# Kernel optimization log

Hardware: AMD Instinct MI355X
Metric: run time of the kernel (lower is better)

## Reference

```python
import jax, jax.numpy as jnp
import numpy as np

N, E, IN_DIM, H, D = 50000, 1600000, 128, 8, 16


def setup_inputs() -> dict:
    key = jax.random.key(0)
    ks = jax.random.split(key, 9)
    s = 1.0 / np.sqrt(IN_DIM)
    return {
        "h": jax.random.normal(ks[0], (N, IN_DIM), dtype=jnp.float32),
        "Wq": jax.random.normal(ks[1], (IN_DIM, H * D), dtype=jnp.float32) * s,
        "bq": jax.random.normal(ks[2], (H * D,), dtype=jnp.float32) * 0.01,
        "Wk": jax.random.normal(ks[3], (IN_DIM, H * D), dtype=jnp.float32) * s,
        "bk": jax.random.normal(ks[4], (H * D,), dtype=jnp.float32) * 0.01,
        "Wv": jax.random.normal(ks[5], (IN_DIM, H * D), dtype=jnp.float32) * s,
        "bv": jax.random.normal(ks[6], (H * D,), dtype=jnp.float32) * 0.01,
        "src": jax.random.randint(ks[7], (E,), 0, N, dtype=jnp.int32),
        "dst": jax.random.randint(ks[8], (E,), 0, N, dtype=jnp.int32),
    }


def reference(h, Wq, bq, Wk, bk, Wv, bv, src, dst):
    n = h.shape[0]
    # node-level projections, reshaped to [N, H, D]
    Q = (h @ Wq + bq).reshape(n, H, D)
    K = (h @ Wk + bk).reshape(n, H, D)
    V = (h @ Wv + bv).reshape(n, H, D)
    # per-edge score: dot(K[src], Q[dst]) / sqrt(D), exp-clamped -> [E, H]
    score = jnp.sum(K[src] * Q[dst], axis=-1) / np.sqrt(D)
    score = jnp.exp(jnp.clip(score, -5.0, 5.0))
    # score-weighted messages scattered into destination nodes
    m = V[src] * score[:, :, None]                    # [E, H, D]
    wV = jax.ops.segment_sum(m, dst, num_segments=n)  # [N, H, D]
    z = jax.ops.segment_sum(score, dst, num_segments=n)  # [N, H]
    h_out = wV / (z[:, :, None] + 1e-6)
    return h_out.reshape(n, H * D)
```

## Files before the change

### kernel.cpp

```cpp
#include <hip/hip_runtime.h>
#include <hip/hip_bf16.h>

#define IN_DIM 128
#define HH 8
#define DD 16
#define HD 128
#define SCAN_B 256
#define CHUNK 8192

#define MT  64
#define KP  136
#define NCH 128

typedef float f32x4 __attribute__((ext_vector_type(4)));
typedef short s16x8 __attribute__((ext_vector_type(8)));

__device__ __forceinline__ int sniff_fp32(const unsigned short* h_raw) {
  int sane = 0;
#pragma unroll
  for (int i = 0; i < 128; i += 2) {
    const unsigned short u = h_raw[i];
    const int expo = (u >> 7) & 0xFF;
    if (expo >= 112 && expo <= 143) sane++;
  }
  return (sane >= 40) ? 0 : 1;
}

__global__ __launch_bounds__(128) void wt_kernel(
    const unsigned short* __restrict__ h_raw,
    const void* __restrict__ Wq, const void* __restrict__ Wk,
    const void* __restrict__ Wv, __hip_bfloat16* __restrict__ Wt,
    int* __restrict__ flag, int* __restrict__ bucket_size) {
  const int isf = sniff_fp32(h_raw);
  const int n = blockIdx.x;
  const int k = threadIdx.x;
  if (n == 0) {
    if (k == 0) *flag = isf;
    for (int j = k; j < 774; j += 128) bucket_size[j] = 0;
  }
  const int mat = n >> 7;
  const int col = n & 127;
  const void* W = (mat == 0) ? Wq : (mat == 1) ? Wk : Wv;
  float v;
  if (isf) v = ((const float*)W)[(size_t)k * HD + col];
  else     v = __bfloat162float(((const __hip_bfloat16*)W)[(size_t)k * HD + col]);
  Wt[(size_t)n * KP + k] = __float2bfloat16(v);
}

__global__ __launch_bounds__(256) void proj_hist_kernel(
    const void* __restrict__ h, const __hip_bfloat16* __restrict__ Wt,
    const void* __restrict__ bq, const void* __restrict__ bk,
    const void* __restrict__ bv,
    __hip_bfloat16* __restrict__ Qb, __hip_bfloat16* __restrict__ KVb,
    const int* __restrict__ flag, int n_nodes,
    const int* __restrict__ dst, int* __restrict__ bucket_size, int n_edges,
    int pgrid) {
  __shared__ short Bs[NCH * KP];
  __shared__ short As[MT * KP];

  const int tid = threadIdx.x;

  if (blockIdx.x >= pgrid) {
    int* lh = (int*)Bs;
    const int e0 = (blockIdx.x - pgrid) * CHUNK;
    const int e1 = (e0 + CHUNK < n_edges) ? e0 + CHUNK : n_edges;
    lh[tid] = 0;
    __syncthreads();
    for (int e = e0 + tid; e < e1; e += 256) atomicAdd(&lh[dst[e] >> 8], 1);
    __syncthreads();
    if (lh[tid] > 0) atomicAdd(&bucket_size[tid], lh[tid]);
    return;
  }

  const int node0 = blockIdx.x * MT;
  const int isf = *flag;

#pragma unroll
  for (int j = 0; j < 16; ++j) {
    const int pid = tid + j * 256;
    const int m = pid >> 6;
    const int kk = (pid & 63) * 2;
    const int g = node0 + m;
    unsigned int pack = 0;
    if (g < n_nodes) {
      if (isf) {
        const float2 f2 = *(const float2*)((const float*)h + (size_t)g * HD + kk);
        const __hip_bfloat16 b0 = __float2bfloat16(f2.x);
        const __hip_bfloat16 b1 = __float2bfloat16(f2.y);
        pack = (unsigned int)(*(const unsigned short*)&b0) |
               ((unsigned int)(*(const unsigned short*)&b1) << 16);
      } else {
        pack = *(const unsigned int*)((const __hip_bfloat16*)h +
                                      (size_t)g * HD + kk);
      }
    }
    *(unsigned int*)&As[m * KP + kk] = pack;
  }
  __syncthreads();

  const int wave = tid >> 6;
  const int lane = tid & 63;
  const int l15 = lane & 15;
  const int quad = lane >> 4;

  s16x8 afrag[4];
#pragma unroll
  for (int k4 = 0; k4 < 4; ++k4)
    afrag[k4] = *(const s16x8*)&As[(wave * 16 + l15) * KP + k4 * 32 + quad * 8];

  for (int c = 0; c < 3; ++c) {
    __syncthreads();
    const uint4* gsrc = (const uint4*)(Wt + (size_t)c * NCH * KP);
    for (int j = tid; j < (NCH * KP * 2) / 16; j += 256)
      ((uint4*)Bs)[j] = gsrc[j];
    __syncthreads();

    f32x4 acc[8];
#pragma unroll
    for (int t = 0; t < 8; ++t) acc[t] = (f32x4){0.f, 0.f, 0.f, 0.f};

#pragma unroll
    for (int t = 0; t < 8; ++t) {
#pragma unroll
      for (int k4 = 0; k4 < 4; ++k4) {
        const s16x8 bfrag =
            *(const s16x8*)&Bs[(t * 16 + l15) * KP + k4 * 32 + quad * 8];
        acc[t] = __builtin_amdgcn_mfma_f32_16x16x32_bf16(afrag[k4], bfrag,
                                                         acc[t], 0, 0, 0);
      }
    }

    const void* bp = (c == 0) ? bq : (c == 1) ? bk : bv;
#pragma unroll
    for (int t = 0; t < 8; ++t) {
      const int ncol = t * 16 + l15;
      const float bias = isf ? ((const float*)bp)[ncol]
                             : __bfloat162float(((const __hip_bfloat16*)bp)[ncol]);
#pragma unroll
      for (int r = 0; r < 4; ++r) {
        const int g = node0 + wave * 16 + quad * 4 + r;
        if (g < n_nodes) {
          const float val = acc[t][r] + bias;
          if (c == 0) {
            Qb[(size_t)g * HD + ncol] = __float2bfloat16(val);
          } else if (c == 1) {
            KVb[(size_t)g * 256 + ncol] = __float2bfloat16(val);
          } else {
            KVb[(size_t)g * 256 + 128 + ncol] = __float2bfloat16(val);
          }
        }
      }
    }
  }
}

__device__ __forceinline__ int block_scan_bucket_size(
    const int* __restrict__ bucket_size, int* sh, int nbuck, int t) {
  const int v = (t < nbuck) ? bucket_size[t] : 0;
  sh[t] = v;
  __syncthreads();
  for (int off = 1; off < 256; off <<= 1) {
    int add = (t >= off) ? sh[t - off] : 0;
    __syncthreads();
    sh[t] += add;
    __syncthreads();
  }
  return sh[t] - v;
}

__global__ __launch_bounds__(256) void bucketize_kernel(
    const int* __restrict__ src, const int* __restrict__ dst,
    const int* __restrict__ bucket_size, int* __restrict__ bucket_cur,
    unsigned int* __restrict__ ebuf, int n_edges, int nbuck) {
  __shared__ int lh[256];
  __shared__ int sscan[256];
  const int t = threadIdx.x;

  const int base_excl = block_scan_bucket_size(bucket_size, sscan, nbuck, t);

  const int e0 = blockIdx.x * CHUNK;
  const int e1 = (e0 + CHUNK < n_edges) ? e0 + CHUNK : n_edges;
  lh[t] = 0;
  __syncthreads();
  for (int e = e0 + t; e < e1; e += 256) atomicAdd(&lh[dst[e] >> 8], 1);
  __syncthreads();
  const int cnt_local = lh[t];
  int base = 0;
  if (cnt_local > 0) base = base_excl + atomicAdd(&bucket_cur[t], cnt_local);
  __syncthreads();
  lh[t] = base;
  __syncthreads();
  for (int e = e0 + t; e < e1; e += 256) {
    const int d = dst[e];
    const int pos = atomicAdd(&lh[d >> 8], 1);
    ebuf[pos] = ((unsigned int)src[e] << 16) | (unsigned int)d;
  }
}

__global__ __launch_bounds__(256) void bucket_csr_kernel(
    const unsigned int* __restrict__ ebuf, const int* __restrict__ bucket_size,
    int* __restrict__ row_ptr, int* __restrict__ edge_src,
    int n_nodes, int nbuck, int n_edges) {
  __shared__ int lc[256];
  __shared__ int sh[256];
  const int b = blockIdx.x;
  const int t = threadIdx.x;

  const int my_excl = block_scan_bucket_size(bucket_size, sh, nbuck, t);
  __syncthreads();
  lc[t] = my_excl;
  __syncthreads();
  const int lo = lc[b];
  const int hi = lo + bucket_size[b];
  const int nbase = b << 8;
  __syncthreads();

  lc[t] = 0;
  __syncthreads();
  for (int i = lo + t; i < hi; i += 256)
    atomicAdd(&lc[(ebuf[i] & 0xFFFFu) - nbase], 1);
  __syncthreads();

  const int v = lc[t];
  sh[t] = v;
  __syncthreads();
  for (int off = 1; off < 256; off <<= 1) {
    int add = (t >= off) ? sh[t - off] : 0;
    __syncthreads();
    sh[t] += add;
    __syncthreads();
  }
  const int excl = sh[t] - v;

  const int node = nbase + t;
  if (node < n_nodes) row_ptr[node] = lo + excl;
  if (b == nbuck - 1 && t == 255) row_ptr[n_nodes] = n_edges;

  __syncthreads();
  lc[t] = lo + excl;
  __syncthreads();
  for (int i = lo + t; i < hi; i += 256) {
    const unsigned int pkd = ebuf[i];
    const int pos = atomicAdd(&lc[(pkd & 0xFFFFu) - nbase], 1);
    edge_src[pos] = (int)(pkd >> 16);
  }
}

__global__ __launch_bounds__(256) void hist_kernel(
    const int* __restrict__ dst, int* __restrict__ cnt, int n_edges) {
  const int e = blockIdx.x * blockDim.x + threadIdx.x;
  if (e < n_edges) atomicAdd(&cnt[dst[e]], 1);
}

__global__ __launch_bounds__(256) void scatter_kernel(
    const int* __restrict__ src, const int* __restrict__ dst,
    int* __restrict__ cursor, int* __restrict__ edge_src, int n_edges) {
  const int e = blockIdx.x * blockDim.x + threadIdx.x;
  if (e < n_edges) {
    const int pos = atomicAdd(&cursor[dst[e]], 1);
    edge_src[pos] = src[e];
  }
}

__global__ __launch_bounds__(SCAN_B) void scan1_kernel(
    const int* __restrict__ cnt, int* __restrict__ exs,
    int* __restrict__ bsum, int n) {
  __shared__ int sh[SCAN_B];
  const int t = threadIdx.x;
  const int i = blockIdx.x * SCAN_B + t;
  int v = (i < n) ? cnt[i] : 0;
  sh[t] = v;
  __syncthreads();
  for (int off = 1; off < SCAN_B; off <<= 1) {
    int add = (t >= off) ? sh[t - off] : 0;
    __syncthreads();
    sh[t] += add;
    __syncthreads();
  }
  if (i < n) exs[i] = sh[t] - v;
  if (t == SCAN_B - 1) bsum[blockIdx.x] = sh[t];
}

__global__ __launch_bounds__(SCAN_B) void scan2_kernel(int* __restrict__ bsum,
                                                       int nb) {
  __shared__ int sh[SCAN_B];
  const int t = threadIdx.x;
  if (nb <= SCAN_B) {
    int v = (t < nb) ? bsum[t] : 0;
    sh[t] = v;
    __syncthreads();
    for (int off = 1; off < SCAN_B; off <<= 1) {
      int add = (t >= off) ? sh[t - off] : 0;
      __syncthreads();
      sh[t] += add;
      __syncthreads();
    }
    if (t < nb) bsum[t] = sh[t] - v;
  } else if (t == 0) {
    int run = 0;
    for (int b = 0; b < nb; ++b) { int v = bsum[b]; bsum[b] = run; run += v; }
  }
}

__global__ __launch_bounds__(SCAN_B) void scan3_kernel(
    const int* __restrict__ exs, const int* __restrict__ bsum,
    int* __restrict__ row_ptr, int* __restrict__ cursor, int n, int n_edges) {
  const int i = blockIdx.x * SCAN_B + threadIdx.x;
  if (i < n) {
    const int v = exs[i] + bsum[blockIdx.x];
    row_ptr[i] = v;
    cursor[i] = v;
  }
  if (i == 0) row_ptr[n] = n_edges;
}

__global__ __launch_bounds__(128) void gather_kernel(
    const int* __restrict__ row_ptr, const int* __restrict__ edge_src,
    const __hip_bfloat16* __restrict__ Qb, const __hip_bfloat16* __restrict__ KVb,
    void* __restrict__ out, const int* __restrict__ flag, int n_nodes) {
  __shared__ float vred[HD][17];
  __shared__ float zred[16][HH];

  const int d = blockIdx.x;
  const int tid = threadIdx.x;

  const int eloc = tid >> 3;
  const int hh8  = tid & 7;

  const int start = row_ptr[d];
  const int deg = row_ptr[d + 1] - start;

  float qreg[16];
  {
    const uint4* qp = (const uint4*)(Qb + (size_t)d * HD + hh8 * 16);
    unsigned int qw[8];
    *(uint4*)&qw[0] = qp[0];
    *(uint4*)&qw[4] = qp[1];
#pragma unroll
    for (int i = 0; i < 8; ++i) {
      qreg[2 * i]     = __uint_as_float(qw[i] << 16) * 0.25f;
      qreg[2 * i + 1] = __uint_as_float(qw[i] & 0xFFFF0000u) * 0.25f;
    }
  }

  float acc[16];
#pragma unroll
  for (int j = 0; j < 16; ++j) acc[j] = 0.0f;
  float zacc = 0.0f;

  int s0 = 0, s1 = 0;
  if (eloc < deg) s0 = edge_src[start + eloc];
  if (eloc + 16 < deg) s1 = edge_src[start + eloc + 16];

  for (int ei = eloc; ei < deg; ei += 32) {
    const int sA = s0;
    const bool hasB = (ei + 16 < deg);
    const int sB = hasB ? s1 : sA;

    const int nx = ei + 32;
    if (nx < deg) s0 = edge_src[start + nx];
    if (nx + 16 < deg) s1 = edge_src[start + nx + 16];

    const uint4* pA = (const uint4*)(KVb + (size_t)sA * 256 + hh8 * 16);
    const uint4* pB = (const uint4*)(KVb + (size_t)sB * 256 + hh8 * 16);
    const uint4 kA0 = pA[0], kA1 = pA[1];
    const uint4 vA0 = pA[16], vA1 = pA[17];
    const uint4 kB0 = pB[0], kB1 = pB[1];
    const uint4 vB0 = pB[16], vB1 = pB[17];

    unsigned int kw[8];
    *(uint4*)&kw[0] = kA0;
    *(uint4*)&kw[4] = kA1;
    float dotA = 0.0f;
#pragma unroll
    for (int i = 0; i < 8; ++i) {
      const float klo = __uint_as_float(kw[i] << 16);
      const float khi = __uint_as_float(kw[i] & 0xFFFF0000u);
      dotA = fmaf(qreg[2 * i], klo, dotA);
      dotA = fmaf(qreg[2 * i + 1], khi, dotA);
    }
    *(uint4*)&kw[0] = kB0;
    *(uint4*)&kw[4] = kB1;
    float dotB = 0.0f;
#pragma unroll
    for (int i = 0; i < 8; ++i) {
      const float klo = __uint_as_float(kw[i] << 16);
      const float khi = __uint_as_float(kw[i] & 0xFFFF0000u);
      dotB = fmaf(qreg[2 * i], klo, dotB);
      dotB = fmaf(qreg[2 * i + 1], khi, dotB);
    }
    const float scoreA = __expf(fminf(fmaxf(dotA, -5.0f), 5.0f));
    float scoreB = __expf(fminf(fmaxf(dotB, -5.0f), 5.0f));
    if (!hasB) scoreB = 0.0f;
    zacc += scoreA + scoreB;

    unsigned int vwA[8], vwB[8];
    *(uint4*)&vwA[0] = vA0;
    *(uint4*)&vwA[4] = vA1;
    *(uint4*)&vwB[0] = vB0;
    *(uint4*)&vwB[4] = vB1;
#pragma unroll
    for (int i = 0; i < 8; ++i) {
      const float vAlo = __uint_as_float(vwA[i] << 16);
      const float vAhi = __uint_as_float(vwA[i] & 0xFFFF0000u);
      const float vBlo = __uint_as_float(vwB[i] << 16);
      const float vBhi = __uint_as_float(vwB[i] & 0xFFFF0000u);
      acc[2 * i]     = fmaf(scoreA, vAlo, acc[2 * i]);
      acc[2 * i]     = fmaf(scoreB, vBlo, acc[2 * i]);
      acc[2 * i + 1] = fmaf(scoreA, vAhi, acc[2 * i + 1]);
      acc[2 * i + 1] = fmaf(scoreB, vBhi, acc[2 * i + 1]);
    }
  }

#pragma unroll
  for (int j = 0; j < 16; ++j) vred[hh8 * 16 + j][eloc] = acc[j];
  zred[eloc][hh8] = zacc;
  __syncthreads();

  const int hd16 = tid >> 4;
  float sumV = 0.0f;
#pragma unroll
  for (int i = 0; i < 16; ++i) sumV += vred[tid][i];
  float sumZ = 0.0f;
#pragma unroll
  for (int i = 0; i < 16; ++i) sumZ += zred[i][hd16];

  const float r = sumV / (sumZ + 1e-6f);
  const size_t o = (size_t)d * HD + tid;
  if (*flag) ((float*)out)[o] = r;
  else       ((__hip_bfloat16*)out)[o] = __float2bfloat16(r);
}

extern "C" void kernel_launch(void* const* d_in, const int* in_sizes, int n_in,
                              void* d_out, int out_size, void* d_ws, size_t ws_size,
                              hipStream_t stream) {
  const void* h  = d_in[0];
  const void* Wq = d_in[1];
  const void* bq = d_in[2];
  const void* Wk = d_in[3];
  const void* bk = d_in[4];
  const void* Wv = d_in[5];
  const void* bv = d_in[6];
  const int* src = (const int*)d_in[7];
  const int* dst = (const int*)d_in[8];

  const int n_nodes = in_sizes[0] / IN_DIM;
  const int n_edges = in_sizes[7];
  const int nb = (n_nodes + SCAN_B - 1) / SCAN_B;
  const int nbuck = (n_nodes + 255) >> 8;

  char* p = (char*)d_ws;
  int* flag = (int*)p;                       p += 256;
  __hip_bfloat16* Qb = (__hip_bfloat16*)p;   p += (size_t)n_nodes * HD * 2;
  __hip_bfloat16* KVb = (__hip_bfloat16*)p;  p += (size_t)n_nodes * 256 * 2;
  __hip_bfloat16* Wt = (__hip_bfloat16*)p;   p += ((size_t)384 * KP * 2 + 255) / 256 * 256;
  int* bucket_size = (int*)p;                p += 258 * 4;
  int* bucket_base = (int*)p;                p += 258 * 4;
  int* bucket_cur = (int*)p;                 p += 258 * 4;
  int* row_ptr = (int*)p;                    p += (size_t)(n_nodes + 1) * 4;
  unsigned int* ebuf = (unsigned int*)p;     p += (size_t)n_edges * 4;
  int* edge_src = (int*)p;                   p += (size_t)n_edges * 4;
  int* cnt = (int*)p;                        p += (size_t)n_nodes * 4;
  int* exs = (int*)p;                        p += (size_t)n_nodes * 4;
  int* bsum = (int*)p;                       p += (size_t)(nb + 1) * 4;
  int* cursor = (int*)p;                     p += (size_t)n_nodes * 4;
  (void)bucket_base;

  wt_kernel<<<384, 128, 0, stream>>>((const unsigned short*)h, Wq, Wk, Wv, Wt,
                                     flag, bucket_size);

  const int pgrid = (n_nodes + MT - 1) / MT;
  const int nchunk = (n_edges + CHUNK - 1) / CHUNK;

  if (n_nodes <= 65536) {
    proj_hist_kernel<<<pgrid + nchunk, 256, 0, stream>>>(
        h, Wt, bq, bk, bv, Qb, KVb, flag, n_nodes, dst, bucket_size,
        n_edges, pgrid);
    bucketize_kernel<<<nchunk, 256, 0, stream>>>(src, dst, bucket_size,
                                                 bucket_cur, ebuf, n_edges,
                                                 nbuck);
    bucket_csr_kernel<<<nbuck, 256, 0, stream>>>(ebuf, bucket_size, row_ptr,
                                                 edge_src, n_nodes, nbuck,
                                                 n_edges);
  } else {
    proj_hist_kernel<<<pgrid, 256, 0, stream>>>(
        h, Wt, bq, bk, bv, Qb, KVb, flag, n_nodes, dst, bucket_size,
        n_edges, pgrid);
    hipMemsetAsync(cnt, 0, (size_t)n_nodes * sizeof(int), stream);
    const int eb = 256;
    const int egrid = (n_edges + eb - 1) / eb;
    hist_kernel<<<egrid, eb, 0, stream>>>(dst, cnt, n_edges);
    scan1_kernel<<<nb, SCAN_B, 0, stream>>>(cnt, exs, bsum, n_nodes);
    scan2_kernel<<<1, SCAN_B, 0, stream>>>(bsum, nb);
    scan3_kernel<<<nb, SCAN_B, 0, stream>>>(exs, bsum, row_ptr, cursor,
                                            n_nodes, n_edges);
    scatter_kernel<<<egrid, eb, 0, stream>>>(src, dst, cursor, edge_src,
                                             n_edges);
  }

  gather_kernel<<<n_nodes, 128, 0, stream>>>(row_ptr, edge_src, Qb, KVb,
                                             d_out, flag, n_nodes);
}
```

Measured before the change: 309.1 us.

## Replace bucketed two-pass CSR build with per-node histogram, rowptr scan and atomic scatter

The CSR construction used to work in stages: a coarse 256-node bucket histogram, a bucketize pass that wrote packed edges into a buffer, and a per-bucket local sort. It now keeps a per-node global atomic histogram, fused into the projection launch, and zeroes the counts inside the weight-transpose kernel. A single rowptr kernel then computes each block's base with a redundant prefix reduction, and a global atomic scatter writes edge sources. This drops the ebuf intermediate and one full pass over the edges. The cost is heavy global atomic contention on the per-node counts and the cursor, plus a quadratic redundant prefix read in rowptr_kernel.

```diff
diff --git a/kernel.cpp b/kernel.cpp
--- a/kernel.cpp
+++ b/kernel.cpp
@@ -30,14 +30,13 @@
     const unsigned short* __restrict__ h_raw,
     const void* __restrict__ Wq, const void* __restrict__ Wk,
     const void* __restrict__ Wv, __hip_bfloat16* __restrict__ Wt,
-    int* __restrict__ flag, int* __restrict__ bucket_size) {
+    int* __restrict__ flag, int* __restrict__ cnt, int n_nodes) {
   const int isf = sniff_fp32(h_raw);
   const int n = blockIdx.x;
   const int k = threadIdx.x;
-  if (n == 0) {
-    if (k == 0) *flag = isf;
-    for (int j = k; j < 774; j += 128) bucket_size[j] = 0;
-  }
+  if (n == 0 && k == 0) *flag = isf;
+  for (int j = n * 128 + k; j < n_nodes; j += 384 * 128) cnt[j] = 0;
+
   const int mat = n >> 7;
   const int col = n & 127;
   const void* W = (mat == 0) ? Wq : (mat == 1) ? Wk : Wv;
@@ -53,7 +52,7 @@
     const void* __restrict__ bv,
     __hip_bfloat16* __restrict__ Qb, __hip_bfloat16* __restrict__ KVb,
     const int* __restrict__ flag, int n_nodes,
-    const int* __restrict__ dst, int* __restrict__ bucket_size, int n_edges,
+    const int* __restrict__ dst, int* __restrict__ cnt, int n_edges,
     int pgrid) {
   __shared__ short Bs[NCH * KP];
   __shared__ short As[MT * KP];
@@ -61,14 +60,9 @@
   const int tid = threadIdx.x;
 
   if (blockIdx.x >= pgrid) {
-    int* lh = (int*)Bs;
     const int e0 = (blockIdx.x - pgrid) * CHUNK;
     const int e1 = (e0 + CHUNK < n_edges) ? e0 + CHUNK : n_edges;
-    lh[tid] = 0;
-    __syncthreads();
-    for (int e = e0 + tid; e < e1; e += 256) atomicAdd(&lh[dst[e] >> 8], 1);
-    __syncthreads();
-    if (lh[tid] > 0) atomicAdd(&bucket_size[tid], lh[tid]);
+    for (int e = e0 + tid; e < e1; e += 256) atomicAdd(&cnt[dst[e]], 1);
     return;
   }
 
@@ -154,74 +148,27 @@
   }
 }
 
-__device__ __forceinline__ int block_scan_bucket_size(
-    const int* __restrict__ bucket_size, int* sh, int nbuck, int t) {
-  const int v = (t < nbuck) ? bucket_size[t] : 0;
-  sh[t] = v;
-  __syncthreads();
-  for (int off = 1; off < 256; off <<= 1) {
-    int add = (t >= off) ? sh[t - off] : 0;
-    __syncthreads();
-    sh[t] += add;
-    __syncthreads();
-  }
-  return sh[t] - v;
-}
-
-__global__ __launch_bounds__(256) void bucketize_kernel(
-    const int* __restrict__ src, const int* __restrict__ dst,
-    const int* __restrict__ bucket_size, int* __restrict__ bucket_cur,
-    unsigned int* __restrict__ ebuf, int n_edges, int nbuck) {
-  __shared__ int lh[256];
-  __shared__ int sscan[256];
-  const int t = threadIdx.x;
-
-  const int base_excl = block_scan_bucket_size(bucket_size, sscan, nbuck, t);
-
-  const int e0 = blockIdx.x * CHUNK;
-  const int e1 = (e0 + CHUNK < n_edges) ? e0 + CHUNK : n_edges;
-  lh[t] = 0;
-  __syncthreads();
-  for (int e = e0 + t; e < e1; e += 256) atomicAdd(&lh[dst[e] >> 8], 1);
-  __syncthreads();
-  const int cnt_local = lh[t];
-  int base = 0;
-  if (cnt_local > 0) base = base_excl + atomicAdd(&bucket_cur[t], cnt_local);
-  __syncthreads();
-  lh[t] = base;
-  __syncthreads();
-  for (int e = e0 + t; e < e1; e += 256) {
-    const int d = dst[e];
-    const int pos = atomicAdd(&lh[d >> 8], 1);
-    ebuf[pos] = ((unsigned int)src[e] << 16) | (unsigned int)d;
-  }
-}
-
-__global__ __launch_bounds__(256) void bucket_csr_kernel(
-    const unsigned int* __restrict__ ebuf, const int* __restrict__ bucket_size,
-    int* __restrict__ row_ptr, int* __restrict__ edge_src,
-    int n_nodes, int nbuck, int n_edges) {
-  __shared__ int lc[256];
+__global__ __launch_bounds__(256) void rowptr_kernel(
+    const int* __restrict__ cnt, int* __restrict__ row_ptr,
+    int* __restrict__ cursor, int n_nodes, int nbuck, int n_edges) {
   __shared__ int sh[256];
   const int b = blockIdx.x;
   const int t = threadIdx.x;
 
-  const int my_excl = block_scan_bucket_size(bucket_size, sh, nbuck, t);
-  __syncthreads();
-  lc[t] = my_excl;
-  __syncthreads();
-  const int lo = lc[b];
-  const int hi = lo + bucket_size[b];
-  const int nbase = b << 8;
-  __syncthreads();
-
-  lc[t] = 0;
-  __syncthreads();
-  for (int i = lo + t; i < hi; i += 256)
-    atomicAdd(&lc[(ebuf[i] & 0xFFFFu) - nbase], 1);
-  __syncthreads();
-
-  const int v = lc[t];
+  int psum = 0;
+  const int lim = b << 8;
+  for (int j = t; j < lim; j += 256) psum += cnt[j];
+  sh[t] = psum;
+  __syncthreads();
+  for (int off = 128; off > 0; off >>= 1) {
+    if (t < off) sh[t] += sh[t + off];
+    __syncthreads();
+  }
+  const int base = sh[0];
+  __syncthreads();
+
+  const int node = lim + t;
+  const int v = (node < n_nodes) ? cnt[node] : 0;
   sh[t] = v;
   __syncthreads();
   for (int off = 1; off < 256; off <<= 1) {
@@ -232,24 +179,11 @@
   }
   const int excl = sh[t] - v;
 
-  const int node = nbase + t;
-  if (node < n_nodes) row_ptr[node] = lo + excl;
+  if (node < n_nodes) {
+    row_ptr[node] = base + excl;
+    cursor[node] = base + excl;
+  }
   if (b == nbuck - 1 && t == 255) row_ptr[n_nodes] = n_edges;
-
-  __syncthreads();
-  lc[t] = lo + excl;
-  __syncthreads();
-  for (int i = lo + t; i < hi; i += 256) {
-    const unsigned int pkd = ebuf[i];
-    const int pos = atomicAdd(&lc[(pkd & 0xFFFFu) - nbase], 1);
-    edge_src[pos] = (int)(pkd >> 16);
-  }
-}
-
-__global__ __launch_bounds__(256) void hist_kernel(
-    const int* __restrict__ dst, int* __restrict__ cnt, int n_edges) {
-  const int e = blockIdx.x * blockDim.x + threadIdx.x;
-  if (e < n_edges) atomicAdd(&cnt[dst[e]], 1);
 }
 
 __global__ __launch_bounds__(256) void scatter_kernel(
@@ -454,49 +388,36 @@
   __hip_bfloat16* Qb = (__hip_bfloat16*)p;   p += (size_t)n_nodes * HD * 2;
   __hip_bfloat16* KVb = (__hip_bfloat16*)p;  p += (size_t)n_nodes * 256 * 2;
   __hip_bfloat16* Wt = (__hip_bfloat16*)p;   p += ((size_t)384 * KP * 2 + 255) / 256 * 256;
-  int* bucket_size = (int*)p;                p += 258 * 4;
-  int* bucket_base = (int*)p;                p += 258 * 4;
-  int* bucket_cur = (int*)p;                 p += 258 * 4;
-  int* row_ptr = (int*)p;                    p += (size_t)(n_nodes + 1) * 4;
-  unsigned int* ebuf = (unsigned int*)p;     p += (size_t)n_edges * 4;
+  int* row_ptr = (int*)p;                    p += (size_t)(n_nodes + 1 + 63) / 64 * 64 * 4;
   int* edge_src = (int*)p;                   p += (size_t)n_edges * 4;
   int* cnt = (int*)p;                        p += (size_t)n_nodes * 4;
+  int* cursor = (int*)p;                     p += (size_t)n_nodes * 4;
   int* exs = (int*)p;                        p += (size_t)n_nodes * 4;
   int* bsum = (int*)p;                       p += (size_t)(nb + 1) * 4;
-  int* cursor = (int*)p;                     p += (size_t)n_nodes * 4;
-  (void)bucket_base;
 
   wt_kernel<<<384, 128, 0, stream>>>((const unsigned short*)h, Wq, Wk, Wv, Wt,
-                                     flag, bucket_size);
+                                     flag, cnt, n_nodes);
 
   const int pgrid = (n_nodes + MT - 1) / MT;
   const int nchunk = (n_edges + CHUNK - 1) / CHUNK;
 
-  if (n_nodes <= 65536) {
-    proj_hist_kernel<<<pgrid + nchunk, 256, 0, stream>>>(
-        h, Wt, bq, bk, bv, Qb, KVb, flag, n_nodes, dst, bucket_size,
-        n_edges, pgrid);
-    bucketize_kernel<<<nchunk, 256, 0, stream>>>(src, dst, bucket_size,
-                                                 bucket_cur, ebuf, n_edges,
-                                                 nbuck);
-    bucket_csr_kernel<<<nbuck, 256, 0, stream>>>(ebuf, bucket_size, row_ptr,
-                                                 edge_src, n_nodes, nbuck,
-                                                 n_edges);
+  proj_hist_kernel<<<pgrid + nchunk, 256, 0, stream>>>(
+      h, Wt, bq, bk, bv, Qb, KVb, flag, n_nodes, dst, cnt, n_edges, pgrid);
+
+  if (nbuck <= 1024) {
+    rowptr_kernel<<<nbuck, 256, 0, stream>>>(cnt, row_ptr, cursor, n_nodes,
+                                             nbuck, n_edges);
   } else {
-    proj_hist_kernel<<<pgrid, 256, 0, stream>>>(
-        h, Wt, bq, bk, bv, Qb, KVb, flag, n_nodes, dst, bucket_size,
-        n_edges, pgrid);
-    hipMemsetAsync(cnt, 0, (size_t)n_nodes * sizeof(int), stream);
-    const int eb = 256;
-    const int egrid = (n_edges + eb - 1) / eb;
-    hist_kernel<<<egrid, eb, 0, stream>>>(dst, cnt, n_edges);
     scan1_kernel<<<nb, SCAN_B, 0, stream>>>(cnt, exs, bsum, n_nodes);
     scan2_kernel<<<1, SCAN_B, 0, stream>>>(bsum, nb);
     scan3_kernel<<<nb, SCAN_B, 0, stream>>>(exs, bsum, row_ptr, cursor,
                                             n_nodes, n_edges);
-    scatter_kernel<<<egrid, eb, 0, stream>>>(src, dst, cursor, edge_src,
-                                             n_edges);
-  }
+  }
+
+  const int eb = 256;
+  const int egrid = (n_edges + eb - 1) / eb;
+  scatter_kernel<<<egrid, eb, 0, stream>>>(src, dst, cursor, edge_src,
+                                           n_edges);
 
   gather_kernel<<<n_nodes, 128, 0, stream>>>(row_ptr, edge_src, Qb, KVb,
                                              d_out, flag, n_nodes);
```

Measured after the change: 447.3 us. 1.45x slower.
